# Performance work log

Hardware: AMD Instinct MI355X
Metric: run time of the kernel (lower is better)

## Reference

```python
import jax, jax.numpy as jnp
import numpy as np

B, S, F, U = 64, 512, 128, 512          # seq_length == units (required for broadcast in original code)
SIGDIM = F + F * F                       # level-2 truncated signature dimension
GRID_SIZE, SPLINE_ORDER = 5, 3           # efficient-KAN style defaults
NB = GRID_SIZE + SPLINE_ORDER            # number of b-spline basis functions per input feature
LN_EPS = 1e-3                            # keras LayerNormalization default epsilon


def _make_grid():
    h = 2.0 / GRID_SIZE  # uniform grid on [-1, 1], extended by spline order
    return -1.0 + h * jnp.arange(-SPLINE_ORDER, GRID_SIZE + SPLINE_ORDER + 1, dtype=jnp.float32)


def _b_splines(x, grid):
    # x: (N, F) -> (N, F, NB) via Cox-de Boor recursion
    x = x[..., None]
    bases = ((x >= grid[:-1]) & (x < grid[1:])).astype(x.dtype)
    for p in range(1, SPLINE_ORDER + 1):
        left = (x - grid[:-(p + 1)]) / (grid[p:-1] - grid[:-(p + 1)])
        right = (grid[p + 1:] - x) / (grid[p + 1:] - grid[1:-p])
        bases = left * bases[..., :-1] + right * bases[..., 1:]
    return bases


def _kan_linear(x, base_w, spline_w, grid):
    # KANLinear, no bias / no layernorm: silu base branch + b-spline branch
    lead = x.shape[:-1]
    base = jax.nn.silu(x) @ base_w                                  # (..., U)
    b = _b_splines(x.reshape(-1, x.shape[-1]), grid)                # (N, F, NB)
    spl = jnp.einsum('nfk,ufk->nu', b, spline_w).reshape(*lead, base_w.shape[1])
    return base + spl


def _signature2(x):
    # level-2 path signature of piecewise-linear path x: (B, S, F) -> (B, F + F*F)
    dx = x[:, 1:] - x[:, :-1]                                       # (B, S-1, F)
    s1 = dx.sum(axis=1)                                             # (B, F)
    cs = jnp.cumsum(dx, axis=1)
    prev = jnp.concatenate([jnp.zeros_like(cs[:, :1]), cs[:, :-1]], axis=1)
    s2 = jnp.einsum('bti,btj->bij', prev + 0.5 * dx, dx)            # (B, F, F)
    return jnp.concatenate([s1, s2.reshape(x.shape[0], -1)], axis=-1)


def _grkan(sig, w1, b1, w2, b2, w3, b3, w4, b4, ws, bs, gamma, beta):
    # gated residual network mapping signature -> softmax attention weights (B, U)
    h = jax.nn.elu(sig @ w1 + b1)
    h = h @ w2 + b2
    glu = jax.nn.sigmoid(h @ w3 + b3) * (h @ w4 + b4)
    y = sig @ ws + bs + glu
    mu = jnp.mean(y, axis=-1, keepdims=True)
    var = jnp.var(y, axis=-1, keepdims=True)
    y = (y - mu) / jnp.sqrt(var + LN_EPS) * gamma + beta
    return jax.nn.softmax(y, axis=-1)


def setup_inputs() -> dict:
    key = jax.random.key(0)
    ks = jax.random.split(key, 24)
    n = lambda k, shp, s=0.02: jax.random.normal(k, shp, dtype=jnp.float32) * s
    inp = {
        'inputs': jax.random.normal(ks[0], (B, S, F), dtype=jnp.float32),
        'h_prev': jax.random.normal(ks[1], (B, U), dtype=jnp.float32),
        'c_prev': jax.random.normal(ks[2], (B, U), dtype=jnp.float32),
        'time_kernel': n(ks[3], (S, 1), 0.1),
        'kan_base_w': n(ks[4], (F, U)),
        'kan_spline_w': n(ks[5], (U, F, NB)),
        'g_w1': n(ks[6], (SIGDIM, U)), 'g_b1': jnp.zeros((U,), jnp.float32),
        'g_w2': n(ks[7], (U, U)), 'g_b2': jnp.zeros((U,), jnp.float32),
        'g_w3': n(ks[8], (U, U)), 'g_b3': jnp.zeros((U,), jnp.float32),
        'g_w4': n(ks[9], (U, U)), 'g_b4': jnp.zeros((U,), jnp.float32),
        'g_skip_w': n(ks[10], (SIGDIM, U)), 'g_skip_b': jnp.zeros((U,), jnp.float32),
        'ln_gamma': jnp.ones((U,), jnp.float32), 'ln_beta': jnp.zeros((U,), jnp.float32),
        'wf': n(ks[11], (2 * U, U)), 'bf': jnp.zeros((U,), jnp.float32),
        'wi': n(ks[12], (2 * U, U)), 'bi': jnp.zeros((U,), jnp.float32),
        'wc': n(ks[13], (2 * U, U)), 'bc': jnp.zeros((U,), jnp.float32),
        'wo': n(ks[14], (2 * U, U)), 'bo': jnp.zeros((U,), jnp.float32),
    }
    return inp


def reference(inputs, h_prev, c_prev, time_kernel, kan_base_w, kan_spline_w,
              g_w1, g_b1, g_w2, g_b2, g_w3, g_b3, g_w4, g_b4, g_skip_w, g_skip_b,
              ln_gamma, ln_beta, wf, bf, wi, bi, wc, bc, wo, bo):
    grid = _make_grid()
    weighted = time_kernel * inputs                                  # (B,S,F)
    sig = _signature2(weighted)                                      # (B,SIGDIM)
    attn = _grkan(sig, g_w1, g_b1, g_w2, g_b2, g_w3, g_b3, g_w4, g_b4,
                  g_skip_w, g_skip_b, ln_gamma, ln_beta)             # (B,S) since U==S
    kan_out = _kan_linear(weighted, kan_base_w, kan_spline_w, grid)  # (B,S,U)
    attended = kan_out * attn[..., None]                             # (B,S,U)
    current = attended.mean(axis=1)                                  # (B,U)
    combined = jnp.concatenate([current, h_prev], axis=-1)           # (B,2U)
    f = jax.nn.sigmoid(combined @ wf + bf)
    i = jax.nn.sigmoid(combined @ wi + bi)
    cand = jnp.tanh(combined @ wc + bc)
    o = jax.nn.sigmoid(combined @ wo + bo)
    c_new = f * c_prev + i * cand
    h_new = o * jnp.tanh(c_new)
    return h_new, c_new
```

## Files before the change

kernel.cpp:

```cpp
#include <hip/hip_runtime.h>
#include <math.h>

#define BB 64
#define SS 512
#define FF 128
#define UU 512
#define NBB 8
#define SIGDIM (FF + FF*FF)
#define K3 16512
#define KK 1152
#define NCH 32

typedef __attribute__((ext_vector_type(8))) __bf16 bf16x8;
typedef __attribute__((ext_vector_type(4))) float f32x4;

__device__ __forceinline__ unsigned short f2bf(float x) {
    unsigned int u = __float_as_uint(x);
    unsigned int r = u + 0x7FFFu + ((u >> 16) & 1u);
    return (unsigned short)(r >> 16);
}

__device__ __forceinline__ float sigmoidf(float x) { return 1.0f / (1.0f + expf(-x)); }

__global__ void k_wprep(const float* __restrict__ splw, const float* __restrict__ basew,
                        const float* __restrict__ h_prev,
                        unsigned short* __restrict__ Wt, unsigned short* __restrict__ comb_b) {
    int idx = blockIdx.x * 256 + threadIdx.x;
    if (idx >= UU * KK) return;
    int u = idx / KK, c = idx % KK;
    float v = (c < 1024) ? splw[(size_t)u * 1024 + c] : basew[(size_t)(c - 1024) * UU + u];
    Wt[idx] = f2bf(v);
    if (idx < BB * UU) {
        int b = idx >> 9, uu = idx & 511;
        comb_b[(size_t)b * 1024 + 512 + uu] = f2bf(h_prev[idx]);
    }
}

__global__ __launch_bounds__(256) void k_wt3(const float* __restrict__ w2, const float* __restrict__ w3,
                                             const float* __restrict__ w4, const float* __restrict__ wf,
                                             const float* __restrict__ wi, const float* __restrict__ wc,
                                             const float* __restrict__ wo,
                                             unsigned short* __restrict__ W2t,
                                             unsigned short* __restrict__ W3t,
                                             unsigned short* __restrict__ W4t,
                                             unsigned short* __restrict__ Wgt) {
    int kt = blockIdx.x, ut = blockIdx.y, z = blockIdx.z;
    int Kdim = (z < 3) ? 512 : 1024;
    if (kt * 64 >= Kdim) return;
    const float* src;
    unsigned short* dst;
    switch (z) {
        case 0: src = w2; dst = W2t; break;
        case 1: src = w3; dst = W3t; break;
        case 2: src = w4; dst = W4t; break;
        case 3: src = wf; dst = Wgt; break;
        case 4: src = wi; dst = Wgt + (size_t)512 * 1024; break;
        case 5: src = wc; dst = Wgt + (size_t)1024 * 1024; break;
        default: src = wo; dst = Wgt + (size_t)1536 * 1024; break;
    }
    __shared__ float tile[64][65];
    int tid = threadIdx.x;
    int k0 = kt * 64, u0 = ut * 64;
#pragma unroll
    for (int p = 0; p < 16; ++p) {
        int e = p * 256 + tid;
        int kk = e >> 6, uu = e & 63;
        tile[kk][uu] = src[(size_t)(k0 + kk) * UU + u0 + uu];
    }
    __syncthreads();
#pragma unroll
    for (int p = 0; p < 16; ++p) {
        int e = p * 256 + tid;
        int uu = e >> 6, kk = e & 63;
        dst[(size_t)(u0 + uu) * Kdim + k0 + kk] = f2bf(tile[kk][uu]);
    }
}

__global__ __launch_bounds__(256) void k_wt2(const float* __restrict__ w1,
                                             const float* __restrict__ gsw,
                                             unsigned short* __restrict__ W1t,
                                             unsigned short* __restrict__ Wst) {
    int kt = blockIdx.x, ut = blockIdx.y, mat = blockIdx.z;
    const float* src = mat ? gsw : w1;
    unsigned short* dst = mat ? Wst : W1t;
    __shared__ float tile[64][65];
    int tid = threadIdx.x;
    int k0 = kt * 64, u0 = ut * 64;
#pragma unroll
    for (int p = 0; p < 16; ++p) {
        int e = p * 256 + tid;
        int kk = e >> 6, uu = e & 63;
        tile[kk][uu] = src[(size_t)(k0 + kk) * UU + u0 + uu];
    }
    __syncthreads();
#pragma unroll
    for (int p = 0; p < 16; ++p) {
        int e = p * 256 + tid;
        int uu = e >> 6, kk = e & 63;
        dst[(size_t)(u0 + uu) * K3 + k0 + kk] = f2bf(tile[kk][uu]);
    }
}

__global__ __launch_bounds__(256) void k_adprep(const float* __restrict__ inp,
                                                const float* __restrict__ tk,
                                                unsigned short* __restrict__ aT,
                                                unsigned short* __restrict__ dT) {
    int tt0 = blockIdx.x * 64, f0 = blockIdx.y * 64, b = blockIdx.z;
    __shared__ float aS[64][65], dS[64][65];
    __shared__ float tkS[65];
    int tid = threadIdx.x;
    if (tid < 65) { int t = tt0 + tid; tkS[tid] = (t < SS) ? tk[t] : 0.f; }
    __syncthreads();
    const float* ib = inp + (size_t)b * SS * FF;
    float tk0 = tk[0];
    for (int e = tid; e < 64 * 64; e += 256) {
        int tt = e >> 6, ff = e & 63;
        int t = tt0 + tt;
        int f = f0 + ff;
        float av = 0.f, dv = 0.f;
        if (t < SS - 1) {
            float wa = tkS[tt] * ib[(size_t)t * FF + f];
            float wn = tkS[tt + 1] * ib[(size_t)(t + 1) * FF + f];
            float w0 = tk0 * ib[f];
            av = 0.5f * (wa + wn) - w0;
            dv = wn - wa;
        }
        aS[tt][ff] = av; dS[tt][ff] = dv;
    }
    __syncthreads();
    for (int e = tid; e < 64 * 64; e += 256) {
        int ff = e >> 6, tt = e & 63;
        size_t o = ((size_t)b * FF + f0 + ff) * SS + tt0 + tt;
        aT[o] = f2bf(aS[tt][ff]);
        dT[o] = f2bf(dS[tt][ff]);
    }
}

__global__ __launch_bounds__(256) void k_sig_mfma(const unsigned short* __restrict__ aT,
                                                  const unsigned short* __restrict__ dT,
                                                  float* __restrict__ s2part) {
    int kc = blockIdx.x, b = blockIdx.y;
    int tid = threadIdx.x, lane = tid & 63;
    int wv = __builtin_amdgcn_readfirstlane(tid >> 6);
    int wrow = (wv & 1) * 64, wcol = (wv >> 1) * 64;
    int k0 = kc * 128;
    const unsigned short* pa = aT + ((size_t)b * FF + wrow + (lane & 15)) * SS + k0 + (lane >> 4) * 8;
    const unsigned short* pd = dT + ((size_t)b * FF + wcol + (lane & 15)) * SS + k0 + (lane >> 4) * 8;
    f32x4 acc[4][4];
#pragma unroll
    for (int i = 0; i < 4; ++i)
#pragma unroll
        for (int j = 0; j < 4; ++j) acc[i][j] = (f32x4)(0.f);
#pragma unroll
    for (int t = 0; t < 4; ++t) {
        bf16x8 af[4], df[4];
#pragma unroll
        for (int rt = 0; rt < 4; ++rt) af[rt] = *(const bf16x8*)(pa + (size_t)rt * 16 * SS + t * 32);
#pragma unroll
        for (int ct = 0; ct < 4; ++ct) df[ct] = *(const bf16x8*)(pd + (size_t)ct * 16 * SS + t * 32);
#pragma unroll
        for (int rt = 0; rt < 4; ++rt)
#pragma unroll
            for (int ct = 0; ct < 4; ++ct)
                acc[rt][ct] = __builtin_amdgcn_mfma_f32_16x16x32_bf16(af[rt], df[ct], acc[rt][ct], 0, 0, 0);
    }
    float* outp = s2part + ((size_t)kc * BB + b) * (FF * FF);
    int quad = lane >> 4, col = lane & 15;
#pragma unroll
    for (int rt = 0; rt < 4; ++rt)
#pragma unroll
        for (int ct = 0; ct < 4; ++ct)
#pragma unroll
            for (int reg = 0; reg < 4; ++reg)
                outp[(wrow + rt * 16 + quad * 4 + reg) * FF + wcol + ct * 16 + col] = acc[rt][ct][reg];
}

__global__ void k_sig_reduce(const float* __restrict__ inp, const float* __restrict__ tk,
                             const float* __restrict__ s2part, unsigned short* __restrict__ sigb) {
    int idx = blockIdx.x * 256 + threadIdx.x;
    if (idx >= BB * SIGDIM) return;
    int b = idx / SIGDIM, r = idx % SIGDIM;
    float v;
    if (r < FF) {
        v = tk[SS - 1] * inp[((size_t)b * SS + SS - 1) * FF + r] - tk[0] * inp[(size_t)b * SS * FF + r];
    } else {
        int ij = r - FF;
        v = 0.f;
#pragma unroll
        for (int c = 0; c < 4; ++c) v += s2part[((size_t)c * BB + b) * (FF * FF) + ij];
    }
    sigb[idx] = f2bf(v);
}

__global__ __launch_bounds__(64) void k_sig_direct(const unsigned short* __restrict__ sigb,
                                                   const unsigned short* __restrict__ W1t,
                                                   const unsigned short* __restrict__ Wst,
                                                   const float* __restrict__ b1,
                                                   unsigned short* __restrict__ h1b,
                                                   float* __restrict__ skippre) {
    int lane = threadIdx.x;
    int mt = blockIdx.x, nt = blockIdx.y, mat = blockIdx.z;
    const unsigned short* Bp = mat ? Wst : W1t;
    const unsigned short* pa = sigb + (size_t)(mt * 16 + (lane & 15)) * K3 + (lane >> 4) * 8;
    const unsigned short* pb = Bp + (size_t)(nt * 16 + (lane & 15)) * K3 + (lane >> 4) * 8;
    f32x4 acc0 = (f32x4)(0.f), acc1 = (f32x4)(0.f);
#pragma unroll 8
    for (int t = 0; t < K3 / 32; t += 2) {
        bf16x8 a0 = *(const bf16x8*)(pa + t * 32);
        bf16x8 b0 = *(const bf16x8*)(pb + t * 32);
        bf16x8 a1 = *(const bf16x8*)(pa + t * 32 + 32);
        bf16x8 b1v = *(const bf16x8*)(pb + t * 32 + 32);
        acc0 = __builtin_amdgcn_mfma_f32_16x16x32_bf16(a0, b0, acc0, 0, 0, 0);
        acc1 = __builtin_amdgcn_mfma_f32_16x16x32_bf16(a1, b1v, acc1, 0, 0, 0);
    }
    int col = lane & 15, quad = lane >> 4;
    int j = nt * 16 + col;
    if (mat == 0) {
        float bb = b1[j];
#pragma unroll
        for (int reg = 0; reg < 4; ++reg) {
            int row = mt * 16 + quad * 4 + reg;
            float v = acc0[reg] + acc1[reg] + bb;
            h1b[(size_t)row * UU + j] = f2bf(v > 0.f ? v : expf(v) - 1.0f);
        }
    } else {
#pragma unroll
        for (int reg = 0; reg < 4; ++reg) {
            int row = mt * 16 + quad * 4 + reg;
            skippre[(size_t)row * UU + j] = acc0[reg] + acc1[reg];
        }
    }
}

__global__ __launch_bounds__(64) void k_h2_direct(const unsigned short* __restrict__ h1b,
                                                  const unsigned short* __restrict__ W2t,
                                                  const float* __restrict__ b2,
                                                  unsigned short* __restrict__ h2b) {
    int lane = threadIdx.x;
    int mt = blockIdx.x, nt = blockIdx.y;
    const unsigned short* pa = h1b + (size_t)(mt * 16 + (lane & 15)) * 512 + (lane >> 4) * 8;
    const unsigned short* pb = W2t + (size_t)(nt * 16 + (lane & 15)) * 512 + (lane >> 4) * 8;
    f32x4 acc0 = (f32x4)(0.f), acc1 = (f32x4)(0.f);
#pragma unroll
    for (int t = 0; t < 16; t += 2) {
        bf16x8 a0 = *(const bf16x8*)(pa + t * 32);
        bf16x8 b0 = *(const bf16x8*)(pb + t * 32);
        bf16x8 a1 = *(const bf16x8*)(pa + t * 32 + 32);
        bf16x8 b1v = *(const bf16x8*)(pb + t * 32 + 32);
        acc0 = __builtin_amdgcn_mfma_f32_16x16x32_bf16(a0, b0, acc0, 0, 0, 0);
        acc1 = __builtin_amdgcn_mfma_f32_16x16x32_bf16(a1, b1v, acc1, 0, 0, 0);
    }
    int col = lane & 15, quad = lane >> 4;
    int j = nt * 16 + col;
    float bb = b2[j];
#pragma unroll
    for (int reg = 0; reg < 4; ++reg) {
        int row = mt * 16 + quad * 4 + reg;
        h2b[(size_t)row * UU + j] = f2bf(acc0[reg] + acc1[reg] + bb);
    }
}

__global__ __launch_bounds__(64) void k_glu_direct(const unsigned short* __restrict__ h2b,
                                                   const unsigned short* __restrict__ W3t,
                                                   const unsigned short* __restrict__ W4t,
                                                   const float* __restrict__ b3,
                                                   const float* __restrict__ b4,
                                                   const float* __restrict__ skippre,
                                                   const float* __restrict__ skb,
                                                   float* __restrict__ yv) {
    int lane = threadIdx.x;
    int mt = blockIdx.x, nt = blockIdx.y;
    const unsigned short* pa = h2b + (size_t)(mt * 16 + (lane & 15)) * 512 + (lane >> 4) * 8;
    const unsigned short* pb3 = W3t + (size_t)(nt * 16 + (lane & 15)) * 512 + (lane >> 4) * 8;
    const unsigned short* pb4 = W4t + (size_t)(nt * 16 + (lane & 15)) * 512 + (lane >> 4) * 8;
    f32x4 acc3 = (f32x4)(0.f), acc4 = (f32x4)(0.f);
#pragma unroll
    for (int t = 0; t < 16; ++t) {
        bf16x8 a = *(const bf16x8*)(pa + t * 32);
        bf16x8 b3f = *(const bf16x8*)(pb3 + t * 32);
        bf16x8 b4f = *(const bf16x8*)(pb4 + t * 32);
        acc3 = __builtin_amdgcn_mfma_f32_16x16x32_bf16(a, b3f, acc3, 0, 0, 0);
        acc4 = __builtin_amdgcn_mfma_f32_16x16x32_bf16(a, b4f, acc4, 0, 0, 0);
    }
    int col = lane & 15, quad = lane >> 4;
    int j = nt * 16 + col;
    float bb3 = b3[j], bb4 = b4[j], sb = skb[j];
#pragma unroll
    for (int reg = 0; reg < 4; ++reg) {
        int row = mt * 16 + quad * 4 + reg;
        float g = sigmoidf(acc3[reg] + bb3);
        yv[(size_t)row * UU + j] = skippre[(size_t)row * UU + j] + sb + g * (acc4[reg] + bb4);
    }
}

__device__ __forceinline__ float block_sum(float v, float* red) {
    int tid = threadIdx.x;
#pragma unroll
    for (int off = 32; off > 0; off >>= 1) v += __shfl_down(v, off);
    __syncthreads();
    if ((tid & 63) == 0) red[tid >> 6] = v;
    __syncthreads();
    float r = red[0];
#pragma unroll
    for (int i = 1; i < 8; ++i) r += red[i];
    return r;
}
__device__ __forceinline__ float block_max(float v, float* red) {
    int tid = threadIdx.x;
#pragma unroll
    for (int off = 32; off > 0; off >>= 1) v = fmaxf(v, __shfl_down(v, off));
    __syncthreads();
    if ((tid & 63) == 0) red[tid >> 6] = v;
    __syncthreads();
    float r = red[0];
#pragma unroll
    for (int i = 1; i < 8; ++i) r = fmaxf(r, red[i]);
    return r;
}

__global__ void k_lnsm(const float* __restrict__ yv, const float* __restrict__ gamma,
                       const float* __restrict__ beta, float* __restrict__ attn) {
    int b = blockIdx.x, u = threadIdx.x;
    __shared__ float red[8];
    float v = yv[(size_t)b * UU + u];
    float mu = block_sum(v, red) * (1.0f / UU);
    float d = v - mu;
    float var = block_sum(d * d, red) * (1.0f / UU);
    float z = d * rsqrtf(var + 1e-3f) * gamma[u] + beta[u];
    float m = block_max(z, red);
    float e = expf(z - m);
    float Z = block_sum(e, red);
    attn[(size_t)b * UU + u] = e / Z;
}

__global__ __launch_bounds__(128) void k_attn_red(const float* __restrict__ inp,
                                                  const float* __restrict__ tk,
                                                  const float* __restrict__ attn,
                                                  float* __restrict__ Apart) {
    int b = blockIdx.x, ch = blockIdx.y;
    int f = threadIdx.x;
    __shared__ float attnS[16], tkS[16];
    if (f < 16) { attnS[f] = attn[(size_t)b * UU + ch * 16 + f]; tkS[f] = tk[ch * 16 + f]; }
    __syncthreads();
    const float* ib = inp + ((size_t)b * SS + ch * 16) * FF + f;
    float acc[9] = {};
#pragma unroll
    for (int s = 0; s < 16; ++s) {
        float w = tkS[s] * ib[(size_t)s * FF];
        float a = attnS[s];
        float t = (w + 2.2f) * 2.5f;
        float cf = floorf(fminf(fmaxf(t, -2.f), 13.f));
        int c = (int)cf;
        float u = t - cf;
        float u2 = u * u, u3 = u2 * u;
        float p0 = u3 * (1.f / 6.f);
        float p1 = (-3.f * u3 + 3.f * u2 + 3.f * u + 1.f) * (1.f / 6.f);
        float p2 = (3.f * u3 - 6.f * u2 + 4.f) * (1.f / 6.f);
        float onemu = 1.f - u;
        float p3 = onemu * onemu * onemu * (1.f / 6.f);
#pragma unroll
        for (int k2 = 0; k2 < 8; ++k2) {
            int d = c - k2;
            float v = (d == 0) ? p0 : (d == 1) ? p1 : (d == 2) ? p2 : (d == 3) ? p3 : 0.f;
            acc[k2] += a * v;
        }
        acc[8] += a * (w * sigmoidf(w));
    }
    float* op = Apart + ((size_t)ch * BB + b) * KK;
    float4 v0 = { acc[0], acc[1], acc[2], acc[3] };
    float4 v1 = { acc[4], acc[5], acc[6], acc[7] };
    *(float4*)(op + f * 8) = v0;
    *(float4*)(op + f * 8 + 4) = v1;
    op[1024 + f] = acc[8];
}

__global__ void k_ared_red(const float* __restrict__ Apart, unsigned short* __restrict__ Aredb) {
    int idx = blockIdx.x * 256 + threadIdx.x;
    if (idx >= BB * KK) return;
    int b = idx / KK, c = idx % KK;
    float s = 0.f;
#pragma unroll
    for (int ch = 0; ch < NCH; ++ch) s += Apart[((size_t)ch * BB + b) * KK + c];
    Aredb[idx] = f2bf(s * (1.0f / SS));
}

__global__ __launch_bounds__(64) void k_cur_direct(const unsigned short* __restrict__ Aredb,
                                                   const unsigned short* __restrict__ Wt,
                                                   unsigned short* __restrict__ comb_b) {
    int lane = threadIdx.x;
    int mt = blockIdx.x, nt = blockIdx.y;
    const unsigned short* pa = Aredb + (size_t)(mt * 16 + (lane & 15)) * KK + (lane >> 4) * 8;
    const unsigned short* pb = Wt + (size_t)(nt * 16 + (lane & 15)) * KK + (lane >> 4) * 8;
    f32x4 acc0 = (f32x4)(0.f), acc1 = (f32x4)(0.f);
#pragma unroll 6
    for (int t = 0; t < KK / 32; t += 2) {
        bf16x8 a0 = *(const bf16x8*)(pa + t * 32);
        bf16x8 b0 = *(const bf16x8*)(pb + t * 32);
        bf16x8 a1 = *(const bf16x8*)(pa + t * 32 + 32);
        bf16x8 b1v = *(const bf16x8*)(pb + t * 32 + 32);
        acc0 = __builtin_amdgcn_mfma_f32_16x16x32_bf16(a0, b0, acc0, 0, 0, 0);
        acc1 = __builtin_amdgcn_mfma_f32_16x16x32_bf16(a1, b1v, acc1, 0, 0, 0);
    }
    int col = lane & 15, quad = lane >> 4;
    int j = nt * 16 + col;
#pragma unroll
    for (int reg = 0; reg < 4; ++reg) {
        int row = mt * 16 + quad * 4 + reg;
        comb_b[(size_t)row * 1024 + j] = f2bf(acc0[reg] + acc1[reg]);
    }
}

__global__ __launch_bounds__(64) void k_gates_direct(const unsigned short* __restrict__ comb_b,
                                                     const unsigned short* __restrict__ Wgt,
                                                     float* __restrict__ gates) {
    int lane = threadIdx.x;
    int mt = blockIdx.x, nt = blockIdx.y;
    const unsigned short* pa = comb_b + (size_t)(mt * 16 + (lane & 15)) * 1024 + (lane >> 4) * 8;
    const unsigned short* pb = Wgt + (size_t)(nt * 16 + (lane & 15)) * 1024 + (lane >> 4) * 8;
    f32x4 acc0 = (f32x4)(0.f), acc1 = (f32x4)(0.f);
#pragma unroll 8
    for (int t = 0; t < 32; t += 2) {
        bf16x8 a0 = *(const bf16x8*)(pa + t * 32);
        bf16x8 b0 = *(const bf16x8*)(pb + t * 32);
        bf16x8 a1 = *(const bf16x8*)(pa + t * 32 + 32);
        bf16x8 b1v = *(const bf16x8*)(pb + t * 32 + 32);
        acc0 = __builtin_amdgcn_mfma_f32_16x16x32_bf16(a0, b0, acc0, 0, 0, 0);
        acc1 = __builtin_amdgcn_mfma_f32_16x16x32_bf16(a1, b1v, acc1, 0, 0, 0);
    }
    int col = lane & 15, quad = lane >> 4;
    int j = nt * 16 + col;
#pragma unroll
    for (int reg = 0; reg < 4; ++reg) {
        int row = mt * 16 + quad * 4 + reg;
        gates[(size_t)row * 2048 + j] = acc0[reg] + acc1[reg];
    }
}

__global__ void k_cell(const float* __restrict__ gates,
                       const float* __restrict__ bf_, const float* __restrict__ bi_,
                       const float* __restrict__ bc_, const float* __restrict__ bo_,
                       const float* __restrict__ c_prev, float* __restrict__ out) {
    int idx = blockIdx.x * 256 + threadIdx.x;
    if (idx >= BB * UU) return;
    int b = idx >> 9, u = idx & 511;
    const float* g = gates + (size_t)b * 2048;
    float f = sigmoidf(g[u] + bf_[u]);
    float ii = sigmoidf(g[512 + u] + bi_[u]);
    float cd = tanhf(g[1024 + u] + bc_[u]);
    float o = sigmoidf(g[1536 + u] + bo_[u]);
    float cn = f * c_prev[idx] + ii * cd;
    out[idx] = o * tanhf(cn);
    out[(size_t)BB * UU + idx] = cn;
}

extern "C" void kernel_launch(void* const* d_in, const int* in_sizes, int n_in,
                              void* d_out, int out_size, void* d_ws, size_t ws_size,
                              hipStream_t stream) {
    const float* inp   = (const float*)d_in[0];
    const float* hprev = (const float*)d_in[1];
    const float* cprev = (const float*)d_in[2];
    const float* tk    = (const float*)d_in[3];
    const float* basew = (const float*)d_in[4];
    const float* splw  = (const float*)d_in[5];
    const float* gw1   = (const float*)d_in[6];
    const float* gb1   = (const float*)d_in[7];
    const float* gw2   = (const float*)d_in[8];
    const float* gb2   = (const float*)d_in[9];
    const float* gw3   = (const float*)d_in[10];
    const float* gb3   = (const float*)d_in[11];
    const float* gw4   = (const float*)d_in[12];
    const float* gb4   = (const float*)d_in[13];
    const float* gsw   = (const float*)d_in[14];
    const float* gsb   = (const float*)d_in[15];
    const float* lng   = (const float*)d_in[16];
    const float* lnb   = (const float*)d_in[17];
    const float* wf    = (const float*)d_in[18];
    const float* bf_   = (const float*)d_in[19];
    const float* wi    = (const float*)d_in[20];
    const float* bi_   = (const float*)d_in[21];
    const float* wc    = (const float*)d_in[22];
    const float* bc_   = (const float*)d_in[23];
    const float* wo    = (const float*)d_in[24];
    const float* bo_   = (const float*)d_in[25];
    float* out = (float*)d_out;

    float* ws = (float*)d_ws;
    size_t o = 0;
    unsigned short* W1t = (unsigned short*)(ws + o); o += (size_t)UU * K3 / 2;
    unsigned short* Wst = (unsigned short*)(ws + o); o += (size_t)UU * K3 / 2;
    unsigned short* Wt  = (unsigned short*)(ws + o); o += (size_t)UU * KK / 2;
    float* s2part   = ws + o; o += (size_t)4 * BB * FF * FF;
    unsigned short* aT = (unsigned short*)(ws + o); o += (size_t)BB * FF * SS / 2;
    unsigned short* dT = (unsigned short*)(ws + o); o += (size_t)BB * FF * SS / 2;
    unsigned short* sigb = (unsigned short*)(ws + o); o += (size_t)BB * K3 / 2;
    float* skippre  = ws + o; o += (size_t)BB * UU;
    unsigned short* h1b = (unsigned short*)(ws + o); o += (size_t)BB * UU / 2;
    unsigned short* h2b = (unsigned short*)(ws + o); o += (size_t)BB * UU / 2;
    float* yv       = ws + o; o += (size_t)BB * UU;
    float* attn     = ws + o; o += (size_t)BB * UU;
    float* Apart    = ws + o; o += (size_t)NCH * BB * KK;
    unsigned short* Aredb = (unsigned short*)(ws + o); o += (size_t)BB * KK / 2;
    unsigned short* W2t = (unsigned short*)(ws + o); o += (size_t)512 * 512 / 2;
    unsigned short* W3t = (unsigned short*)(ws + o); o += (size_t)512 * 512 / 2;
    unsigned short* W4t = (unsigned short*)(ws + o); o += (size_t)512 * 512 / 2;
    unsigned short* Wgt = (unsigned short*)(ws + o); o += (size_t)2048 * 1024 / 2;
    unsigned short* comb_b = (unsigned short*)(ws + o); o += (size_t)BB * 1024 / 2;
    float* gates    = ws + o; o += (size_t)BB * 2048;
    (void)ws_size; (void)in_sizes; (void)n_in; (void)out_size;

    k_wprep<<<(UU * KK + 255) / 256, 256, 0, stream>>>(splw, basew, hprev, Wt, comb_b);
    k_wt3<<<dim3(16, 8, 7), 256, 0, stream>>>(gw2, gw3, gw4, wf, wi, wc, wo, W2t, W3t, W4t, Wgt);
    k_wt2<<<dim3(K3 / 64, UU / 64, 2), 256, 0, stream>>>(gw1, gsw, W1t, Wst);
    k_adprep<<<dim3(8, 2, BB), 256, 0, stream>>>(inp, tk, aT, dT);
    k_sig_mfma<<<dim3(4, BB), 256, 0, stream>>>(aT, dT, s2part);
    k_sig_reduce<<<(BB * SIGDIM + 255) / 256, 256, 0, stream>>>(inp, tk, s2part, sigb);
    k_sig_direct<<<dim3(4, 32, 2), 64, 0, stream>>>(sigb, W1t, Wst, gb1, h1b, skippre);
    k_h2_direct<<<dim3(4, 32), 64, 0, stream>>>(h1b, W2t, gb2, h2b);
    k_glu_direct<<<dim3(4, 32), 64, 0, stream>>>(h2b, W3t, W4t, gb3, gb4, skippre, gsb, yv);
    k_lnsm<<<BB, UU, 0, stream>>>(yv, lng, lnb, attn);
    k_attn_red<<<dim3(BB, NCH), 128, 0, stream>>>(inp, tk, attn, Apart);
    k_ared_red<<<(BB * KK + 255) / 256, 256, 0, stream>>>(Apart, Aredb);
    k_cur_direct<<<dim3(4, 32), 64, 0, stream>>>(Aredb, Wt, comb_b);
    k_gates_direct<<<dim3(4, 128), 64, 0, stream>>>(comb_b, Wgt, gates);
    k_cell<<<(BB * UU + 255) / 256, 256, 0, stream>>>(gates, bf_, bi_, bc_, bo_, cprev, out);
}
```

Baseline: 298.0 us.

## Merge prep kernels, fuse signature reduce, atomic attn reduce, fuse LSTM gates and cell

The four weight and activation prep kernels become one launch that dispatches on block id. The level-2 signature GEMM now runs over the full time axis per batch and writes bf16 directly, which removes the partial buffer and its reduce kernel. The attention-weighted spline reduction accumulates into a zeroed buffer (apparently with LDS staging and atomics), dropping the Apart partials and their reduce kernel. The gate GEMM and LSTM cell math are fused into one kernel, cutting launches and intermediate traffic at the cost of less parallelism in the signature kernel (64 blocks) and atomic contention.

```diff
diff --git a/kernel.cpp b/kernel.cpp
--- a/kernel.cpp
+++ b/kernel.cpp
@@ -5,14 +5,21 @@
 #define SS 512
 #define FF 128
 #define UU 512
-#define NBB 8
 #define SIGDIM (FF + FF*FF)
 #define K3 16512
 #define KK 1152
 #define NCH 32
 
+#define NB_WT2 4128
+#define NB_WT3 896
+#define NB_AD  1024
+#define NB_WP  2304
+#define NB_PREP (NB_WT2 + NB_WT3 + NB_AD + NB_WP)
+
 typedef __attribute__((ext_vector_type(8))) __bf16 bf16x8;
 typedef __attribute__((ext_vector_type(4))) float f32x4;
+
+union BFPACK { unsigned short s[8]; bf16x8 v; };
 
 __device__ __forceinline__ unsigned short f2bf(float x) {
     unsigned int u = __float_as_uint(x);
@@ -22,137 +29,151 @@
 
 __device__ __forceinline__ float sigmoidf(float x) { return 1.0f / (1.0f + expf(-x)); }
 
-__global__ void k_wprep(const float* __restrict__ splw, const float* __restrict__ basew,
-                        const float* __restrict__ h_prev,
-                        unsigned short* __restrict__ Wt, unsigned short* __restrict__ comb_b) {
-    int idx = blockIdx.x * 256 + threadIdx.x;
-    if (idx >= UU * KK) return;
-    int u = idx / KK, c = idx % KK;
-    float v = (c < 1024) ? splw[(size_t)u * 1024 + c] : basew[(size_t)(c - 1024) * UU + u];
-    Wt[idx] = f2bf(v);
-    if (idx < BB * UU) {
-        int b = idx >> 9, uu = idx & 511;
-        comb_b[(size_t)b * 1024 + 512 + uu] = f2bf(h_prev[idx]);
-    }
-}
-
-__global__ __launch_bounds__(256) void k_wt3(const float* __restrict__ w2, const float* __restrict__ w3,
-                                             const float* __restrict__ w4, const float* __restrict__ wf,
-                                             const float* __restrict__ wi, const float* __restrict__ wc,
-                                             const float* __restrict__ wo,
-                                             unsigned short* __restrict__ W2t,
-                                             unsigned short* __restrict__ W3t,
-                                             unsigned short* __restrict__ W4t,
-                                             unsigned short* __restrict__ Wgt) {
-    int kt = blockIdx.x, ut = blockIdx.y, z = blockIdx.z;
-    int Kdim = (z < 3) ? 512 : 1024;
-    if (kt * 64 >= Kdim) return;
-    const float* src;
-    unsigned short* dst;
-    switch (z) {
-        case 0: src = w2; dst = W2t; break;
-        case 1: src = w3; dst = W3t; break;
-        case 2: src = w4; dst = W4t; break;
-        case 3: src = wf; dst = Wgt; break;
-        case 4: src = wi; dst = Wgt + (size_t)512 * 1024; break;
-        case 5: src = wc; dst = Wgt + (size_t)1024 * 1024; break;
-        default: src = wo; dst = Wgt + (size_t)1536 * 1024; break;
-    }
-    __shared__ float tile[64][65];
-    int tid = threadIdx.x;
-    int k0 = kt * 64, u0 = ut * 64;
-#pragma unroll
-    for (int p = 0; p < 16; ++p) {
-        int e = p * 256 + tid;
-        int kk = e >> 6, uu = e & 63;
-        tile[kk][uu] = src[(size_t)(k0 + kk) * UU + u0 + uu];
-    }
-    __syncthreads();
-#pragma unroll
-    for (int p = 0; p < 16; ++p) {
-        int e = p * 256 + tid;
-        int uu = e >> 6, kk = e & 63;
-        dst[(size_t)(u0 + uu) * Kdim + k0 + kk] = f2bf(tile[kk][uu]);
-    }
-}
-
-__global__ __launch_bounds__(256) void k_wt2(const float* __restrict__ w1,
-                                             const float* __restrict__ gsw,
-                                             unsigned short* __restrict__ W1t,
-                                             unsigned short* __restrict__ Wst) {
-    int kt = blockIdx.x, ut = blockIdx.y, mat = blockIdx.z;
-    const float* src = mat ? gsw : w1;
-    unsigned short* dst = mat ? Wst : W1t;
-    __shared__ float tile[64][65];
-    int tid = threadIdx.x;
-    int k0 = kt * 64, u0 = ut * 64;
-#pragma unroll
-    for (int p = 0; p < 16; ++p) {
-        int e = p * 256 + tid;
-        int kk = e >> 6, uu = e & 63;
-        tile[kk][uu] = src[(size_t)(k0 + kk) * UU + u0 + uu];
-    }
-    __syncthreads();
-#pragma unroll
-    for (int p = 0; p < 16; ++p) {
-        int e = p * 256 + tid;
-        int uu = e >> 6, kk = e & 63;
-        dst[(size_t)(u0 + uu) * K3 + k0 + kk] = f2bf(tile[kk][uu]);
-    }
-}
-
-__global__ __launch_bounds__(256) void k_adprep(const float* __restrict__ inp,
-                                                const float* __restrict__ tk,
-                                                unsigned short* __restrict__ aT,
-                                                unsigned short* __restrict__ dT) {
-    int tt0 = blockIdx.x * 64, f0 = blockIdx.y * 64, b = blockIdx.z;
-    __shared__ float aS[64][65], dS[64][65];
-    __shared__ float tkS[65];
-    int tid = threadIdx.x;
-    if (tid < 65) { int t = tt0 + tid; tkS[tid] = (t < SS) ? tk[t] : 0.f; }
-    __syncthreads();
-    const float* ib = inp + (size_t)b * SS * FF;
-    float tk0 = tk[0];
-    for (int e = tid; e < 64 * 64; e += 256) {
-        int tt = e >> 6, ff = e & 63;
-        int t = tt0 + tt;
-        int f = f0 + ff;
-        float av = 0.f, dv = 0.f;
-        if (t < SS - 1) {
-            float wa = tkS[tt] * ib[(size_t)t * FF + f];
-            float wn = tkS[tt + 1] * ib[(size_t)(t + 1) * FF + f];
-            float w0 = tk0 * ib[f];
-            av = 0.5f * (wa + wn) - w0;
-            dv = wn - wa;
-        }
-        aS[tt][ff] = av; dS[tt][ff] = dv;
-    }
-    __syncthreads();
-    for (int e = tid; e < 64 * 64; e += 256) {
-        int ff = e >> 6, tt = e & 63;
-        size_t o = ((size_t)b * FF + f0 + ff) * SS + tt0 + tt;
-        aT[o] = f2bf(aS[tt][ff]);
-        dT[o] = f2bf(dS[tt][ff]);
-    }
-}
-
-__global__ __launch_bounds__(256) void k_sig_mfma(const unsigned short* __restrict__ aT,
-                                                  const unsigned short* __restrict__ dT,
-                                                  float* __restrict__ s2part) {
-    int kc = blockIdx.x, b = blockIdx.y;
+__global__ __launch_bounds__(256) void k_prep(
+        const float* __restrict__ inp, const float* __restrict__ tk,
+        const float* __restrict__ splw, const float* __restrict__ basew,
+        const float* __restrict__ hprev,
+        const float* __restrict__ gw1, const float* __restrict__ gsw,
+        const float* __restrict__ gw2, const float* __restrict__ gw3,
+        const float* __restrict__ gw4, const float* __restrict__ wf,
+        const float* __restrict__ wi, const float* __restrict__ wc,
+        const float* __restrict__ wo,
+        unsigned short* __restrict__ aT, unsigned short* __restrict__ dT,
+        unsigned short* __restrict__ Wt, unsigned short* __restrict__ comb_b,
+        unsigned short* __restrict__ W1t, unsigned short* __restrict__ Wst,
+        unsigned short* __restrict__ W2t, unsigned short* __restrict__ W3t,
+        unsigned short* __restrict__ W4t, unsigned short* __restrict__ Wgt) {
+    __shared__ float sh[2 * 64 * 65 + 66];
+    int id = blockIdx.x, tid = threadIdx.x;
+
+    if (id < NB_WT2) {
+        int mat = id / (NB_WT2 / 2);
+        int rem = id % (NB_WT2 / 2);
+        int kt = rem >> 3, ut = rem & 7;
+        const float* src = mat ? gsw : gw1;
+        unsigned short* dst = mat ? Wst : W1t;
+        float* tile = sh;
+        int k0 = kt * 64, u0 = ut * 64;
+#pragma unroll
+        for (int p = 0; p < 16; ++p) {
+            int e = p * 256 + tid;
+            int kk = e >> 6, uu = e & 63;
+            tile[kk * 65 + uu] = src[(size_t)(k0 + kk) * UU + u0 + uu];
+        }
+        __syncthreads();
+#pragma unroll
+        for (int p = 0; p < 16; ++p) {
+            int e = p * 256 + tid;
+            int uu = e >> 6, kk = e & 63;
+            dst[(size_t)(u0 + uu) * K3 + k0 + kk] = f2bf(tile[kk * 65 + uu]);
+        }
+        return;
+    }
+    if (id < NB_WT2 + NB_WT3) {
+        int id2 = id - NB_WT2;
+        int z = id2 >> 7;
+        int rem = id2 & 127;
+        int kt = rem >> 3, ut = rem & 7;
+        int Kdim = (z < 3) ? 512 : 1024;
+        if (kt * 64 >= Kdim) return;
+        const float* src;
+        unsigned short* dst;
+        switch (z) {
+            case 0: src = gw2; dst = W2t; break;
+            case 1: src = gw3; dst = W3t; break;
+            case 2: src = gw4; dst = W4t; break;
+            case 3: src = wf; dst = Wgt; break;
+            case 4: src = wi; dst = Wgt + (size_t)512 * 1024; break;
+            case 5: src = wc; dst = Wgt + (size_t)1024 * 1024; break;
+            default: src = wo; dst = Wgt + (size_t)1536 * 1024; break;
+        }
+        float* tile = sh;
+        int k0 = kt * 64, u0 = ut * 64;
+#pragma unroll
+        for (int p = 0; p < 16; ++p) {
+            int e = p * 256 + tid;
+            int kk = e >> 6, uu = e & 63;
+            tile[kk * 65 + uu] = src[(size_t)(k0 + kk) * UU + u0 + uu];
+        }
+        __syncthreads();
+#pragma unroll
+        for (int p = 0; p < 16; ++p) {
+            int e = p * 256 + tid;
+            int uu = e >> 6, kk = e & 63;
+            dst[(size_t)(u0 + uu) * Kdim + k0 + kk] = f2bf(tile[kk * 65 + uu]);
+        }
+        return;
+    }
+    if (id < NB_WT2 + NB_WT3 + NB_AD) {
+        int id3 = id - NB_WT2 - NB_WT3;
+        int b = id3 & 63, ft = (id3 >> 6) & 1, tt = id3 >> 7;
+        int tt0 = tt * 64, f0 = ft * 64;
+        float* aS = sh;
+        float* dS = sh + 64 * 65;
+        float* tkS = sh + 2 * 64 * 65;
+        if (tid < 65) { int t = tt0 + tid; tkS[tid] = (t < SS) ? tk[t] : 0.f; }
+        __syncthreads();
+        const float* ib = inp + (size_t)b * SS * FF;
+        float tk0 = tk[0];
+        for (int e = tid; e < 64 * 64; e += 256) {
+            int ttl = e >> 6, ff = e & 63;
+            int t = tt0 + ttl;
+            int f = f0 + ff;
+            float av = 0.f, dv = 0.f;
+            if (t < SS - 1) {
+                float wa = tkS[ttl] * ib[(size_t)t * FF + f];
+                float wn = tkS[ttl + 1] * ib[(size_t)(t + 1) * FF + f];
+                float w0 = tk0 * ib[f];
+                av = 0.5f * (wa + wn) - w0;
+                dv = wn - wa;
+            }
+            aS[ttl * 65 + ff] = av; dS[ttl * 65 + ff] = dv;
+        }
+        __syncthreads();
+        for (int e = tid; e < 64 * 64; e += 256) {
+            int ff = e >> 6, ttl = e & 63;
+            size_t o = ((size_t)b * FF + f0 + ff) * SS + tt0 + ttl;
+            aT[o] = f2bf(aS[ttl * 65 + ff]);
+            dT[o] = f2bf(dS[ttl * 65 + ff]);
+        }
+        return;
+    }
+    {
+        int idx = (id - NB_WT2 - NB_WT3 - NB_AD) * 256 + tid;
+        if (idx >= UU * KK) return;
+        int u = idx / KK, c = idx % KK;
+        float v = (c < 1024) ? splw[(size_t)u * 1024 + c] : basew[(size_t)(c - 1024) * UU + u];
+        Wt[idx] = f2bf(v);
+        if (idx < BB * UU) {
+            int b = idx >> 9, uu = idx & 511;
+            comb_b[(size_t)b * 1024 + 512 + uu] = f2bf(hprev[idx]);
+        }
+    }
+}
+
+__global__ __launch_bounds__(256) void k_sig_fused(const unsigned short* __restrict__ aT,
+                                                   const unsigned short* __restrict__ dT,
+                                                   const float* __restrict__ inp,
+                                                   const float* __restrict__ tk,
+                                                   unsigned short* __restrict__ sigb) {
+    int b = blockIdx.x;
     int tid = threadIdx.x, lane = tid & 63;
     int wv = __builtin_amdgcn_readfirstlane(tid >> 6);
+    if (tid < 128) {
+        const float* ib = inp + (size_t)b * SS * FF;
+        float v = tk[SS - 1] * ib[(size_t)(SS - 1) * FF + tid] - tk[0] * ib[tid];
+        sigb[(size_t)b * K3 + tid] = f2bf(v);
+    }
     int wrow = (wv & 1) * 64, wcol = (wv >> 1) * 64;
-    int k0 = kc * 128;
-    const unsigned short* pa = aT + ((size_t)b * FF + wrow + (lane & 15)) * SS + k0 + (lane >> 4) * 8;
-    const unsigned short* pd = dT + ((size_t)b * FF + wcol + (lane & 15)) * SS + k0 + (lane >> 4) * 8;
+    const unsigned short* pa = aT + ((size_t)b * FF + wrow + (lane & 15)) * SS + (lane >> 4) * 8;
+    const unsigned short* pd = dT + ((size_t)b * FF + wcol + (lane & 15)) * SS + (lane >> 4) * 8;
     f32x4 acc[4][4];
 #pragma unroll
     for (int i = 0; i < 4; ++i)
 #pragma unroll
         for (int j = 0; j < 4; ++j) acc[i][j] = (f32x4)(0.f);
-#pragma unroll
-    for (int t = 0; t < 4; ++t) {
+#pragma unroll 4
+    for (int t = 0; t < 16; ++t) {
         bf16x8 af[4], df[4];
 #pragma unroll
         for (int rt = 0; rt < 4; ++rt) af[rt] = *(const bf16x8*)(pa + (size_t)rt * 16 * SS + t * 32);
@@ -164,7 +185,7 @@
             for (int ct = 0; ct < 4; ++ct)
                 acc[rt][ct] = __builtin_amdgcn_mfma_f32_16x16x32_bf16(af[rt], df[ct], acc[rt][ct], 0, 0, 0);
     }
-    float* outp = s2part + ((size_t)kc * BB + b) * (FF * FF);
+    unsigned short* op = sigb + (size_t)b * K3 + 128;
     int quad = lane >> 4, col = lane & 15;
 #pragma unroll
     for (int rt = 0; rt < 4; ++rt)
@@ -172,24 +193,8 @@
         for (int ct = 0; ct < 4; ++ct)
 #pragma unroll
             for (int reg = 0; reg < 4; ++reg)
-                outp[(wrow + rt * 16 + quad * 4 + reg) * FF + wcol + ct * 16 + col] = acc[rt][ct][reg];
-}
-
-__global__ void k_sig_reduce(const float* __restrict__ inp, const float* __restrict__ tk,
-                             const float* __restrict__ s2part, unsigned short* __restrict__ sigb) {
-    int idx = blockIdx.x * 256 + threadIdx.x;
-    if (idx >= BB * SIGDIM) return;
-    int b = idx / SIGDIM, r = idx % SIGDIM;
-    float v;
-    if (r < FF) {
-        v = tk[SS - 1] * inp[((size_t)b * SS + SS - 1) * FF + r] - tk[0] * inp[(size_t)b * SS * FF + r];
-    } else {
-        int ij = r - FF;
-        v = 0.f;
-#pragma unroll
-        for (int c = 0; c < 4; ++c) v += s2part[((size_t)c * BB + b) * (FF * FF) + ij];
-    }
-    sigb[idx] = f2bf(v);
+                op[(size_t)(wrow + rt * 16 + quad * 4 + reg) * FF + wcol + ct * 16 + col] =
+                    f2bf(acc[rt][ct][reg]);
 }
 
 __global__ __launch_bounds__(64) void k_sig_direct(const unsigned short* __restrict__ sigb,
@@ -319,8 +324,11 @@
 }
 
 __global__ void k_lnsm(const float* __restrict__ yv, const float* __restrict__ gamma,
-                       const float* __restrict__ beta, float* __restrict__ attn) {
+                       const float* __restrict__ beta, float* __restrict__ attn,
+                       float* __restrict__ Ared) {
     int b = blockIdx.x, u = threadIdx.x;
+    int gid = b * UU + u;
+    for (int i = gid; i < BB * KK; i += BB * UU) Ared[i] = 0.f;
     __shared__ float red[8];
     float v = yv[(size_t)b * UU + u];
     float mu = block_sum(v, red) * (1.0f / UU);
@@ -336,14 +344,18 @@
 __global__ __launch_bounds__(128) void k_attn_red(const float* __restrict__ inp,
                                                   const float* __restrict__ tk,
                                                   const float* __restrict__ attn,
-                                                  float* __restrict__ Apart) {
+                                                  float* __restrict__ Ared) {
     int b = blockIdx.x, ch = blockIdx.y;
-    int f = threadIdx.x;
+    int tid = threadIdx.x;
     __shared__ float attnS[16], tkS[16];
-    if (f < 16) { attnS[f] = attn[(size_t)b * UU + ch * 16 + f]; tkS[f] = tk[ch * 16 + f]; }
+    __shared__ float lacc[128 * 9];
+    float* myacc = lacc + tid * 9;
+#pragma unroll
+    for (int j = 0; j < 8; ++j) myacc[j] = 0.f;
+    if (tid < 16) { attnS[tid] = attn[(size_t)b * UU + ch * 16 + tid]; tkS[tid] = tk[ch * 16 + tid]; }
     __syncthreads();
-    const float* ib = inp + ((size_t)b * SS + ch * 16) * FF + f;
-    float acc[9] = {};
+    const float* ib = inp + ((size_t)b * SS + ch * 16) * FF + tid;
+    float accS = 0.f;
 #pragma unroll
     for (int s = 0; s < 16; ++s) {
         float w = tkS[s] * ib[(size_t)s * FF];
@@ -353,104 +365,98 @@
         int c = (int)cf;
         float u = t - cf;
         float u2 = u * u, u3 = u2 * u;
-        float p0 = u3 * (1.f / 6.f);
-        float p1 = (-3.f * u3 + 3.f * u2 + 3.f * u + 1.f) * (1.f / 6.f);
-        float p2 = (3.f * u3 - 6.f * u2 + 4.f) * (1.f / 6.f);
+        float p[4];
+        p[0] = u3 * (1.f / 6.f);
+        p[1] = (-3.f * u3 + 3.f * u2 + 3.f * u + 1.f) * (1.f / 6.f);
+        p[2] = (3.f * u3 - 6.f * u2 + 4.f) * (1.f / 6.f);
         float onemu = 1.f - u;
-        float p3 = onemu * onemu * onemu * (1.f / 6.f);
-#pragma unroll
-        for (int k2 = 0; k2 < 8; ++k2) {
-            int d = c - k2;
-            float v = (d == 0) ? p0 : (d == 1) ? p1 : (d == 2) ? p2 : (d == 3) ? p3 : 0.f;
-            acc[k2] += a * v;
-        }
-        acc[8] += a * (w * sigmoidf(w));
-    }
-    float* op = Apart + ((size_t)ch * BB + b) * KK;
-    float4 v0 = { acc[0], acc[1], acc[2], acc[3] };
-    float4 v1 = { acc[4], acc[5], acc[6], acc[7] };
-    *(float4*)(op + f * 8) = v0;
-    *(float4*)(op + f * 8 + 4) = v1;
-    op[1024 + f] = acc[8];
-}
-
-__global__ void k_ared_red(const float* __restrict__ Apart, unsigned short* __restrict__ Aredb) {
-    int idx = blockIdx.x * 256 + threadIdx.x;
-    if (idx >= BB * KK) return;
-    int b = idx / KK, c = idx % KK;
-    float s = 0.f;
-#pragma unroll
-    for (int ch = 0; ch < NCH; ++ch) s += Apart[((size_t)ch * BB + b) * KK + c];
-    Aredb[idx] = f2bf(s * (1.0f / SS));
-}
-
-__global__ __launch_bounds__(64) void k_cur_direct(const unsigned short* __restrict__ Aredb,
+        p[3] = onemu * onemu * onemu * (1.f / 6.f);
+#pragma unroll
+        for (int j = 0; j < 4; ++j) {
+            int k2 = c - j;
+            bool ok = (k2 >= 0) && (k2 < 8);
+            int ka = ok ? k2 : 0;
+            float val = ok ? a * p[j] : 0.f;
+            myacc[ka] += val;
+        }
+        accS += a * (w * sigmoidf(w));
+    }
+    float* op = Ared + (size_t)b * KK;
+#pragma unroll
+    for (int j = 0; j < 8; ++j) atomicAdd(op + tid * 8 + j, myacc[j]);
+    atomicAdd(op + 1024 + tid, accS);
+}
+
+__global__ __launch_bounds__(64) void k_cur_direct(const float* __restrict__ Ared,
                                                    const unsigned short* __restrict__ Wt,
                                                    unsigned short* __restrict__ comb_b) {
     int lane = threadIdx.x;
     int mt = blockIdx.x, nt = blockIdx.y;
-    const unsigned short* pa = Aredb + (size_t)(mt * 16 + (lane & 15)) * KK + (lane >> 4) * 8;
+    const float* pa = Ared + (size_t)(mt * 16 + (lane & 15)) * KK + (lane >> 4) * 8;
     const unsigned short* pb = Wt + (size_t)(nt * 16 + (lane & 15)) * KK + (lane >> 4) * 8;
-    f32x4 acc0 = (f32x4)(0.f), acc1 = (f32x4)(0.f);
+    const float sc = 1.0f / SS;
+    f32x4 acc0 = (f32x4)(0.f);
 #pragma unroll 6
-    for (int t = 0; t < KK / 32; t += 2) {
-        bf16x8 a0 = *(const bf16x8*)(pa + t * 32);
-        bf16x8 b0 = *(const bf16x8*)(pb + t * 32);
-        bf16x8 a1 = *(const bf16x8*)(pa + t * 32 + 32);
-        bf16x8 b1v = *(const bf16x8*)(pb + t * 32 + 32);
-        acc0 = __builtin_amdgcn_mfma_f32_16x16x32_bf16(a0, b0, acc0, 0, 0, 0);
-        acc1 = __builtin_amdgcn_mfma_f32_16x16x32_bf16(a1, b1v, acc1, 0, 0, 0);
+    for (int t = 0; t < KK / 32; ++t) {
+        float4 f0 = *(const float4*)(pa + t * 32);
+        float4 f1 = *(const float4*)(pa + t * 32 + 4);
+        BFPACK ap;
+        ap.s[0] = f2bf(f0.x * sc); ap.s[1] = f2bf(f0.y * sc);
+        ap.s[2] = f2bf(f0.z * sc); ap.s[3] = f2bf(f0.w * sc);
+        ap.s[4] = f2bf(f1.x * sc); ap.s[5] = f2bf(f1.y * sc);
+        ap.s[6] = f2bf(f1.z * sc); ap.s[7] = f2bf(f1.w * sc);
+        bf16x8 bfr = *(const bf16x8*)(pb + t * 32);
+        acc0 = __builtin_amdgcn_mfma_f32_16x16x32_bf16(ap.v, bfr, acc0, 0, 0, 0);
     }
     int col = lane & 15, quad = lane >> 4;
     int j = nt * 16 + col;
 #pragma unroll
     for (int reg = 0; reg < 4; ++reg) {
         int row = mt * 16 + quad * 4 + reg;
-        comb_b[(size_t)row * 1024 + j] = f2bf(acc0[reg] + acc1[reg]);
-    }
-}
-
-__global__ __launch_bounds__(64) void k_gates_direct(const unsigned short* __restrict__ comb_b,
-                                                     const unsigned short* __restrict__ Wgt,
-                                                     float* __restrict__ gates) {
+        comb_b[(size_t)row * 1024 + j] = f2bf(acc0[reg]);
+    }
+}
+
+__global__ __launch_bounds__(64) void k_lstm_direct(const unsigned short* __restrict__ comb_b,
+                                                    const unsigned short* __restrict__ Wgt,
+                                                    const float* __restrict__ bf_,
+                                                    const float* __restrict__ bi_,
+                                                    const float* __restrict__ bc_,
+                                                    const float* __restrict__ bo_,
+                                                    const float* __restrict__ c_prev,
+                                                    float* __restrict__ out) {
     int lane = threadIdx.x;
-    int mt = blockIdx.x, nt = blockIdx.y;
+    int mt = blockIdx.x, ut = blockIdx.y;
     const unsigned short* pa = comb_b + (size_t)(mt * 16 + (lane & 15)) * 1024 + (lane >> 4) * 8;
-    const unsigned short* pb = Wgt + (size_t)(nt * 16 + (lane & 15)) * 1024 + (lane >> 4) * 8;
-    f32x4 acc0 = (f32x4)(0.f), acc1 = (f32x4)(0.f);
+    size_t brow = (size_t)(ut * 16 + (lane & 15)) * 1024 + (lane >> 4) * 8;
+    const unsigned short* pbF = Wgt + brow;
+    const unsigned short* pbI = Wgt + (size_t)512 * 1024 + brow;
+    const unsigned short* pbC = Wgt + (size_t)1024 * 1024 + brow;
+    const unsigned short* pbO = Wgt + (size_t)1536 * 1024 + brow;
+    f32x4 aF = (f32x4)(0.f), aI = (f32x4)(0.f), aC = (f32x4)(0.f), aO = (f32x4)(0.f);
 #pragma unroll 8
-    for (int t = 0; t < 32; t += 2) {
-        bf16x8 a0 = *(const bf16x8*)(pa + t * 32);
-        bf16x8 b0 = *(const bf16x8*)(pb + t * 32);
-        bf16x8 a1 = *(const bf16x8*)(pa + t * 32 + 32);
-        bf16x8 b1v = *(const bf16x8*)(pb + t * 32 + 32);
-        acc0 = __builtin_amdgcn_mfma_f32_16x16x32_bf16(a0, b0, acc0, 0, 0, 0);
-        acc1 = __builtin_amdgcn_mfma_f32_16x16x32_bf16(a1, b1v, acc1, 0, 0, 0);
+    for (int t = 0; t < 32; ++t) {
+        bf16x8 a = *(const bf16x8*)(pa + t * 32);
+        aF = __builtin_amdgcn_mfma_f32_16x16x32_bf16(a, *(const bf16x8*)(pbF + t * 32), aF, 0, 0, 0);
+        aI = __builtin_amdgcn_mfma_f32_16x16x32_bf16(a, *(const bf16x8*)(pbI + t * 32), aI, 0, 0, 0);
+        aC = __builtin_amdgcn_mfma_f32_16x16x32_bf16(a, *(const bf16x8*)(pbC + t * 32), aC, 0, 0, 0);
+        aO = __builtin_amdgcn_mfma_f32_16x16x32_bf16(a, *(const bf16x8*)(pbO + t * 32), aO, 0, 0, 0);
     }
     int col = lane & 15, quad = lane >> 4;
-    int j = nt * 16 + col;
+    int j = ut * 16 + col;
+    float bF = bf_[j], bI = bi_[j], bC = bc_[j], bO = bo_[j];
 #pragma unroll
     for (int reg = 0; reg < 4; ++reg) {
         int row = mt * 16 + quad * 4 + reg;
-        gates[(size_t)row * 2048 + j] = acc0[reg] + acc1[reg];
-    }
-}
-
-__global__ void k_cell(const float* __restrict__ gates,
-                       const float* __restrict__ bf_, const float* __restrict__ bi_,
-                       const float* __restrict__ bc_, const float* __restrict__ bo_,
-                       const float* __restrict__ c_prev, float* __restrict__ out) {
-    int idx = blockIdx.x * 256 + threadIdx.x;
-    if (idx >= BB * UU) return;
-    int b = idx >> 9, u = idx & 511;
-    const float* g = gates + (size_t)b * 2048;
-    float f = sigmoidf(g[u] + bf_[u]);
-    float ii = sigmoidf(g[512 + u] + bi_[u]);
-    float cd = tanhf(g[1024 + u] + bc_[u]);
-    float o = sigmoidf(g[1536 + u] + bo_[u]);
-    float cn = f * c_prev[idx] + ii * cd;
-    out[idx] = o * tanhf(cn);
-    out[(size_t)BB * UU + idx] = cn;
+        size_t o = (size_t)row * UU + j;
+        float f = sigmoidf(aF[reg] + bF);
+        float ii = sigmoidf(aI[reg] + bI);
+        float cd = tanhf(aC[reg] + bC);
+        float oo = sigmoidf(aO[reg] + bO);
+        float cn = f * c_prev[o] + ii * cd;
+        out[o] = oo * tanhf(cn);
+        out[(size_t)BB * UU + o] = cn;
+    }
 }
 
 extern "C" void kernel_launch(void* const* d_in, const int* in_sizes, int n_in,
@@ -489,7 +495,6 @@
     unsigned short* W1t = (unsigned short*)(ws + o); o += (size_t)UU * K3 / 2;
     unsigned short* Wst = (unsigned short*)(ws + o); o += (size_t)UU * K3 / 2;
     unsigned short* Wt  = (unsigned short*)(ws + o); o += (size_t)UU * KK / 2;
-    float* s2part   = ws + o; o += (size_t)4 * BB * FF * FF;
     unsigned short* aT = (unsigned short*)(ws + o); o += (size_t)BB * FF * SS / 2;
     unsigned short* dT = (unsigned short*)(ws + o); o += (size_t)BB * FF * SS / 2;
     unsigned short* sigb = (unsigned short*)(ws + o); o += (size_t)BB * K3 / 2;
@@ -498,29 +503,23 @@
     unsigned short* h2b = (unsigned short*)(ws + o); o += (size_t)BB * UU / 2;
     float* yv       = ws + o; o += (size_t)BB * UU;
     float* attn     = ws + o; o += (size_t)BB * UU;
-    float* Apart    = ws + o; o += (size_t)NCH * BB * KK;
-    unsigned short* Aredb = (unsigned short*)(ws + o); o += (size_t)BB * KK / 2;
+    float* Ared     = ws + o; o += (size_t)BB * KK;
     unsigned short* W2t = (unsigned short*)(ws + o); o += (size_t)512 * 512 / 2;
     unsigned short* W3t = (unsigned short*)(ws + o); o += (size_t)512 * 512 / 2;
     unsigned short* W4t = (unsigned short*)(ws + o); o += (size_t)512 * 512 / 2;
     unsigned short* Wgt = (unsigned short*)(ws + o); o += (size_t)2048 * 1024 / 2;
     unsigned short* comb_b = (unsigned short*)(ws + o); o += (size_t)BB * 1024 / 2;
-    float* gates    = ws + o; o += (size_t)BB * 2048;
     (void)ws_size; (void)in_sizes; (void)n_in; (void)out_size;
 
-    k_wprep<<<(UU * KK + 255) / 256, 256, 0, stream>>>(splw, basew, hprev, Wt, comb_b);
-    k_wt3<<<dim3(16, 8, 7), 256, 0, stream>>>(gw2, gw3, gw4, wf, wi, wc, wo, W2t, W3t, W4t, Wgt);
-    k_wt2<<<dim3(K3 / 64, UU / 64, 2), 256, 0, stream>>>(gw1, gsw, W1t, Wst);
-    k_adprep<<<dim3(8, 2, BB), 256, 0, stream>>>(inp, tk, aT, dT);
-    k_sig_mfma<<<dim3(4, BB), 256, 0, stream>>>(aT, dT, s2part);
-    k_sig_reduce<<<(BB * SIGDIM + 255) / 256, 256, 0, stream>>>(inp, tk, s2part, sigb);
+    k_prep<<<NB_PREP, 256, 0, stream>>>(inp, tk, splw, basew, hprev, gw1, gsw, gw2, gw3, gw4,
+                                        wf, wi, wc, wo, aT, dT, Wt, comb_b,
+                                        W1t, Wst, W2t, W3t, W4t, Wgt);
+    k_sig_fused<<<BB, 256, 0, stream>>>(aT, dT, inp, tk, sigb);
     k_sig_direct<<<dim3(4, 32, 2), 64, 0, stream>>>(sigb, W1t, Wst, gb1, h1b, skippre);
     k_h2_direct<<<dim3(4, 32), 64, 0, stream>>>(h1b, W2t, gb2, h2b);
     k_glu_direct<<<dim3(4, 32), 64, 0, stream>>>(h2b, W3t, W4t, gb3, gb4, skippre, gsb, yv);
-    k_lnsm<<<BB, UU, 0, stream>>>(yv, lng, lnb, attn);
-    k_attn_red<<<dim3(BB, NCH), 128, 0, stream>>>(inp, tk, attn, Apart);
-    k_ared_red<<<(BB * KK + 255) / 256, 256, 0, stream>>>(Apart, Aredb);
-    k_cur_direct<<<dim3(4, 32), 64, 0, stream>>>(Aredb, Wt, comb_b);
-    k_gates_direct<<<dim3(4, 128), 64, 0, stream>>>(comb_b, Wgt, gates);
-    k_cell<<<(BB * UU + 255) / 256, 256, 0, stream>>>(gates, bf_, bi_, bc_, bo_, cprev, out);
-}
+    k_lnsm<<<BB, UU, 0, stream>>>(yv, lng, lnb, attn, Ared);
+    k_attn_red<<<dim3(BB, NCH), 128, 0, stream>>>(inp, tk, attn, Ared);
+    k_cur_direct<<<dim3(4, 32), 64, 0, stream>>>(Ared, Wt, comb_b);
+    k_lstm_direct<<<dim3(4, 32), 64, 0, stream>>>(comb_b, Wgt, bf_, bi_, bc_, bo_, cprev, out);
+}
```

Result: slower. 346.0 us (+16.1%).
